# Optimization experiments

Measured on AMD Instinct MI355X. Metric: run time of the kernel, lower is better.

The kernel has to match this reference:

```python
import jax, jax.numpy as jnp
import numpy as np

NUM_HEADS = 16
ROTARY_BASE = 10000.0


def _rope_cos_sin(seqlen, rotary_dim, dtype):
    # inv_freq: (rotary_dim/2,), cos/sin: (seqlen, rotary_dim/2)
    inv_freq = 1.0 / (ROTARY_BASE ** (jnp.arange(0, rotary_dim, 2, dtype=jnp.float32) / rotary_dim))
    t = jnp.arange(seqlen, dtype=jnp.float32)
    freqs = jnp.outer(t, inv_freq)
    return jnp.cos(freqs).astype(dtype), jnp.sin(freqs).astype(dtype)


def _apply_rotary(x, cos, sin):
    # x: (b, s, h, d); cos/sin: (s, d/2). Non-interleaved (GPT-NeoX) halves.
    d2 = cos.shape[-1]
    x1, x2 = x[..., :d2], x[..., d2:2 * d2]
    c = cos[None, :, None, :]
    s = sin[None, :, None, :]
    r1 = x1 * c - x2 * s
    r2 = x1 * s + x2 * c
    return jnp.concatenate([r1, r2], axis=-1)


def setup_inputs() -> dict:
    key = jax.random.key(0)
    ks = jax.random.split(key, 5)
    B, S, E = 2, 2048, 2048
    x = jax.random.normal(ks[0], (B, S, E), dtype=jnp.float32)
    wqkv_w = jax.random.normal(ks[1], (3 * E, E), dtype=jnp.float32) * 0.02
    wqkv_b = jax.random.normal(ks[2], (3 * E,), dtype=jnp.float32) * 0.02
    out_w = jax.random.normal(ks[3], (E, E), dtype=jnp.float32) * 0.02
    out_b = jax.random.normal(ks[4], (E,), dtype=jnp.float32) * 0.02
    return {"x": x, "wqkv_w": wqkv_w, "wqkv_b": wqkv_b, "out_w": out_w, "out_b": out_b}


def reference(x, wqkv_w, wqkv_b, out_w, out_b):
    B, S, E = x.shape
    H = NUM_HEADS
    D = E // H
    # fused QKV projection: (b, s, 3, h, d)
    qkv = (jnp.einsum('bse,fe->bsf', x, wqkv_w) + wqkv_b).reshape(B, S, 3, H, D)
    q, k, v = qkv[:, :, 0], qkv[:, :, 1], qkv[:, :, 2]
    # rotary embedding on full head_dim of q and k
    cos, sin = _rope_cos_sin(S, D, x.dtype)
    q = _apply_rotary(q, cos, sin)
    k = _apply_rotary(k, cos, sin)
    # causal self-attention, softmax_scale = 1/sqrt(head_dim)
    scale = 1.0 / jnp.sqrt(jnp.asarray(D, dtype=x.dtype))
    scores = jnp.einsum('bshd,bthd->bhst', q, k) * scale
    causal_mask = jnp.tril(jnp.ones((S, S), dtype=bool))
    scores = jnp.where(causal_mask[None, None], scores, jnp.asarray(-1e30, dtype=scores.dtype))
    attn = jax.nn.softmax(scores, axis=-1)
    ctx = jnp.einsum('bhst,bthd->bshd', attn, v).reshape(B, S, E)
    return jnp.einsum('bse,fe->bsf', ctx, out_w) + out_b
```

## Files before the change

### kernel.cpp

```cpp
#include <hip/hip_runtime.h>

typedef unsigned short u16;
typedef unsigned int u32;
typedef __bf16 bf16x8 __attribute__((ext_vector_type(8)));
typedef float fx4 __attribute__((ext_vector_type(4)));

__device__ __forceinline__ float bf2f(u16 u) {
    return __uint_as_float(((u32)u) << 16);
}
__device__ __forceinline__ u16 f2bf(float f) {
    u32 x = __float_as_uint(f);
    u32 r = (x + 0x7fffu + ((x >> 16) & 1u)) >> 16;
    return (u16)r;
}

__device__ __forceinline__ void gld16(const u16* g, u16* l) {
    __builtin_amdgcn_global_load_lds(
        (const __attribute__((address_space(1))) void*)g,
        (__attribute__((address_space(3))) void*)l, 16, 0, 0);
}

#define MFMA16(a, b, c) __builtin_amdgcn_mfma_f32_16x16x32_bf16((a), (b), (c), 0, 0, 0)

__global__ __launch_bounds__(256) void cvt_kernel(const float* __restrict__ x,
                                                  const float* __restrict__ w1,
                                                  const float* __restrict__ w2,
                                                  u16* __restrict__ xb,
                                                  u16* __restrict__ w1b,
                                                  u16* __restrict__ w2b) {
    size_t g = ((size_t)blockIdx.x * 256 + threadIdx.x) * 8;
    const float* src;
    u16* dst;
    if (g < 8388608) {
        src = x;
        dst = xb;
    } else if (g < 20971520) {
        src = w1 - 8388608;
        dst = w1b - 8388608;
    } else {
        src = w2 - 20971520;
        dst = w2b - 20971520;
    }
    float4 a = *(const float4*)&src[g];
    float4 b = *(const float4*)&src[g + 4];
    u16 v[8];
    v[0] = f2bf(a.x);
    v[1] = f2bf(a.y);
    v[2] = f2bf(a.z);
    v[3] = f2bf(a.w);
    v[4] = f2bf(b.x);
    v[5] = f2bf(b.y);
    v[6] = f2bf(b.z);
    v[7] = f2bf(b.w);
    *(uint4*)&dst[g] = *(const uint4*)v;
}

template <int MODE>
__global__ __launch_bounds__(256, 2) void gemm_bt(const u16* __restrict__ A,
                                                  const u16* __restrict__ B,
                                                  const float* __restrict__ bias,
                                                  float* __restrict__ Cf,
                                                  u16* __restrict__ qb,
                                                  u16* __restrict__ kb,
                                                  u16* __restrict__ vb,
                                                  int N, int K) {
    __shared__ __align__(16) u16 As[128 * 32];
    __shared__ __align__(16) u16 Bs[128 * 32];

    const int tid = threadIdx.x;
    const int lane = tid & 63;
    const int wave = tid >> 6;
    const int quad = lane >> 4;
    const int m16 = lane & 15;
    const int wm = wave >> 1, wn = wave & 1;
    const int bm = blockIdx.y * 128, bn = blockIdx.x * 128;

    const int r0 = tid >> 2;
    const int u0 = (tid & 3) ^ ((r0 >> 1) & 3);
    const int r1 = (tid + 256) >> 2;
    const int u1 = ((tid + 256) & 3) ^ ((r1 >> 1) & 3);
    const u16* a0 = &A[(size_t)(bm + r0) * K + u0 * 8];
    const u16* a1 = &A[(size_t)(bm + r1) * K + u1 * 8];
    const u16* b0 = &B[(size_t)(bn + r0) * K + u0 * 8];
    const u16* b1 = &B[(size_t)(bn + r1) * K + u1 * 8];
    u16* la0 = &As[tid * 8];
    u16* la1 = &As[(tid + 256) * 8];
    u16* lb0 = &Bs[tid * 8];
    u16* lb1 = &Bs[(tid + 256) * 8];

    const int su = (quad ^ ((m16 >> 1) & 3)) * 8;

    const fx4 zero4 = {0.f, 0.f, 0.f, 0.f};
    fx4 acc[4][4];
#pragma unroll
    for (int i = 0; i < 4; ++i)
#pragma unroll
        for (int j = 0; j < 4; ++j) acc[i][j] = zero4;

    const int nk = K >> 5;
    for (int kt = 0; kt < nk; ++kt) {
        const int k0 = kt << 5;
        gld16(a0 + k0, la0);
        gld16(a1 + k0, la1);
        gld16(b0 + k0, lb0);
        gld16(b1 + k0, lb1);
        __syncthreads();
        bf16x8 af[4], bfr[4];
#pragma unroll
        for (int t = 0; t < 4; ++t) {
            af[t] = *(const bf16x8*)&As[(wm * 64 + t * 16 + m16) * 32 + su];
            bfr[t] = *(const bf16x8*)&Bs[(wn * 64 + t * 16 + m16) * 32 + su];
        }
#pragma unroll
        for (int mt = 0; mt < 4; ++mt)
#pragma unroll
            for (int nt = 0; nt < 4; ++nt)
                acc[mt][nt] = MFMA16(af[mt], bfr[nt], acc[mt][nt]);
        __syncthreads();
    }

#pragma unroll
    for (int mt = 0; mt < 4; ++mt) {
#pragma unroll
        for (int r = 0; r < 4; ++r) {
            int row = bm + wm * 64 + mt * 16 + quad * 4 + r;
#pragma unroll
            for (int nt = 0; nt < 4; ++nt) {
                int col = bn + wn * 64 + nt * 16 + m16;
                float v = acc[mt][nt][r] + bias[col];
                if (MODE == 0) {
                    Cf[(size_t)row * N + col] = v;
                } else {
                    int which = col >> 11;
                    int h = (col >> 7) & 15;
                    int d = col & 127;
                    int b = row >> 11;
                    int s = row & 2047;
                    u16* dst = (which == 0) ? qb : ((which == 1) ? kb : vb);
                    dst[(size_t)((b * 16 + h) * 2048 + s) * 128 + d] = f2bf(v);
                }
            }
        }
    }
}

__global__ __launch_bounds__(256) void rope_kernel(u16* __restrict__ q,
                                                   u16* __restrict__ k) {
    int t = blockIdx.x * 256 + threadIdx.x;
    int i = t & 63;
    int s = (t >> 6) & 2047;
    int bh = t >> 17;
    float inv = exp2f(-(float)i * 0.2076205059304595f);
    float ang = (float)s * inv;
    float sn, cs;
    sincosf(ang, &sn, &cs);
    size_t base = ((size_t)bh * 2048 + s) * 128 + i;
    {
        float x1 = bf2f(q[base]), x2 = bf2f(q[base + 64]);
        q[base] = f2bf(x1 * cs - x2 * sn);
        q[base + 64] = f2bf(x1 * sn + x2 * cs);
    }
    {
        float x1 = bf2f(k[base]), x2 = bf2f(k[base + 64]);
        k[base] = f2bf(x1 * cs - x2 * sn);
        k[base + 64] = f2bf(x1 * sn + x2 * cs);
    }
}

__global__ __launch_bounds__(256) void vtrans_kernel(const u16* __restrict__ v,
                                                     u16* __restrict__ vt) {
    __shared__ __align__(16) u16 L[128 * 66];
    const int tid = threadIdx.x;
    const int kb = blockIdx.x * 64;
    const int bh = blockIdx.y;
    const u16* vp = v + (size_t)bh * 2048 * 128;
    u16* op = vt + (size_t)bh * 128 * 2048;
#pragma unroll
    for (int i = 0; i < 4; ++i) {
        int c = i * 256 + tid;
        int t = c >> 4, d8 = (c & 15) << 3;
        uint4 x = *(const uint4*)&vp[(kb + t) * 128 + d8];
        const u16* xs = (const u16*)&x;
#pragma unroll
        for (int j = 0; j < 8; ++j) L[(d8 + j) * 66 + t] = xs[j];
    }
    __syncthreads();
#pragma unroll
    for (int i = 0; i < 4; ++i) {
        int c = i * 256 + tid;
        int d = c >> 3, t8 = (c & 7) << 3;
        uint4 x;
        u16* xs = (u16*)&x;
#pragma unroll
        for (int j = 0; j < 8; ++j) xs[j] = L[d * 66 + t8 + j];
        *(uint4*)&op[(size_t)d * 2048 + kb + t8] = x;
    }
}

__global__ __launch_bounds__(256, 2) void attn_kernel(const u16* __restrict__ q,
                                                      const u16* __restrict__ k,
                                                      const u16* __restrict__ vt,
                                                      u16* __restrict__ ctx) {
    __shared__ __align__(16) u16 Ks[64 * 128];
    __shared__ __align__(16) u16 Vs[128 * 64];
    __shared__ __align__(16) u16 Ps[4][16 * 64];

    const int tid = threadIdx.x;
    const int lane = tid & 63;
    const int wave = tid >> 6;
    const int quad = lane >> 4;
    const int m16 = lane & 15;

    const int l = blockIdx.x;
    const int a_ = l & 7;
    const int t_ = (l >> 3) & 1;
    const int e_ = (l >> 4) & 1;
    const int d_ = l >> 5;
    const int b_ = t_ ^ (d_ >> 3);
    const int qt_raw = a_ | (e_ << 3);
    const int qt = b_ ? (15 - qt_raw) : qt_raw;
    const int bh = d_ | (t_ << 4);
    const int b = bh >> 4, h = bh & 15;
    const int qbase = qt * 128;
    const u16* qp = q + (size_t)bh * 2048 * 128;
    const u16* kp = k + (size_t)bh * 2048 * 128;
    const u16* vp = vt + (size_t)bh * 128 * 2048;
    const float scale = 0.08838834764831845f;

    bf16x8 qf[2][4];
#pragma unroll
    for (int f = 0; f < 2; ++f)
#pragma unroll
        for (int c = 0; c < 4; ++c)
            qf[f][c] =
                *(const bf16x8*)&qp[(size_t)(qbase + wave * 32 + f * 16 + m16) *
                                        128 +
                                    c * 32 + quad * 8];

    const fx4 zero4 = {0.f, 0.f, 0.f, 0.f};
    fx4 o[2][8];
#pragma unroll
    for (int f = 0; f < 2; ++f)
#pragma unroll
        for (int i = 0; i < 8; ++i) o[f][i] = zero4;
    float mi[2][4], li[2][4];
#pragma unroll
    for (int f = 0; f < 2; ++f)
#pragma unroll
        for (int r = 0; r < 4; ++r) {
            mi[f][r] = -1e30f;
            li[f][r] = 0.f;
        }

    uint4 kr[4], vr[4];
    const int st_t = tid >> 4, st_d8 = (tid & 15) << 3;
    const int st_dv = tid >> 3, st_t8 = (tid & 7) << 3;

#define LOAD_TILE(kb_)                                                        \
    {                                                                         \
        _Pragma("unroll") for (int ii = 0; ii < 4; ++ii) {                    \
            kr[ii] = *(const uint4*)&kp[(size_t)((kb_) + st_t + ii * 16) *    \
                                            128 +                             \
                                        st_d8];                               \
            vr[ii] = *(const uint4*)&vp[(size_t)(st_dv + ii * 32) * 2048 +    \
                                        (kb_) + st_t8];                       \
        }                                                                     \
    }

#define STORE_TILE()                                                          \
    {                                                                         \
        _Pragma("unroll") for (int ii = 0; ii < 4; ++ii) {                    \
            int tt = st_t + ii * 16;                                          \
            int eK = tt * 128 + st_d8;                                        \
            *(uint4*)&Ks[eK ^ ((tt & 7) << 3)] = kr[ii];                      \
            int dv = st_dv + ii * 32;                                         \
            int eV = dv * 64 + st_t8;                                         \
            *(uint4*)&Vs[eV ^ ((dv & 7) << 3)] = vr[ii];                      \
        }                                                                     \
    }

    const int nkt = 2 * qt + 2;
    LOAD_TILE(0);
    for (int kt = 0; kt < nkt; ++kt) {
        const int kb = kt * 64;
        STORE_TILE();
        __syncthreads();
        if (kt + 1 < nkt) LOAD_TILE(kb + 64);

#pragma unroll
        for (int f = 0; f < 2; ++f) {
            fx4 sc[4];
#pragma unroll
            for (int nt = 0; nt < 4; ++nt) sc[nt] = zero4;
#pragma unroll
            for (int c = 0; c < 4; ++c)
#pragma unroll
                for (int nt = 0; nt < 4; ++nt) {
                    int e = (nt * 16 + m16) * 128 + c * 32 + quad * 8;
                    bf16x8 kf = *(const bf16x8*)&Ks[e ^ ((m16 & 7) << 3)];
                    sc[nt] = MFMA16(qf[f][c], kf, sc[nt]);
                }

#pragma unroll
            for (int r = 0; r < 4; ++r) {
                int rg = qbase + wave * 32 + f * 16 + quad * 4 + r;
                float mx = mi[f][r];
#pragma unroll
                for (int nt = 0; nt < 4; ++nt) {
                    int cg = kb + nt * 16 + m16;
                    float s = sc[nt][r] * scale;
                    s = (cg <= rg) ? s : -1e30f;
                    sc[nt][r] = s;
                    mx = fmaxf(mx, s);
                }
                mx = fmaxf(mx, __shfl_xor(mx, 1));
                mx = fmaxf(mx, __shfl_xor(mx, 2));
                mx = fmaxf(mx, __shfl_xor(mx, 4));
                mx = fmaxf(mx, __shfl_xor(mx, 8));
                float alpha = __expf(mi[f][r] - mx);
                mi[f][r] = mx;
                float rsum = 0.f;
                int row = quad * 4 + r;
#pragma unroll
                for (int nt = 0; nt < 4; ++nt) {
                    float p = __expf(sc[nt][r] - mx);
                    Ps[wave][(row * 64 + nt * 16 + m16) ^ ((row & 7) << 3)] =
                        f2bf(p);
                    rsum += p;
                }
                rsum += __shfl_xor(rsum, 1);
                rsum += __shfl_xor(rsum, 2);
                rsum += __shfl_xor(rsum, 4);
                rsum += __shfl_xor(rsum, 8);
                li[f][r] = li[f][r] * alpha + rsum;
#pragma unroll
                for (int dn = 0; dn < 8; ++dn) o[f][dn][r] *= alpha;
            }

#pragma unroll
            for (int c2 = 0; c2 < 2; ++c2) {
                bf16x8 pf = *(const bf16x8*)&Ps[wave][(m16 * 64 + c2 * 32 +
                                                       quad * 8) ^
                                                      ((m16 & 7) << 3)];
#pragma unroll
                for (int dn = 0; dn < 8; ++dn) {
                    int e = (dn * 16 + m16) * 64 + c2 * 32 + quad * 8;
                    bf16x8 vf = *(const bf16x8*)&Vs[e ^ ((m16 & 7) << 3)];
                    o[f][dn] = MFMA16(pf, vf, o[f][dn]);
                }
            }
        }
        __syncthreads();
    }

#pragma unroll
    for (int f = 0; f < 2; ++f)
#pragma unroll
        for (int r = 0; r < 4; ++r) {
            int row = qbase + wave * 32 + f * 16 + quad * 4 + r;
            float inv = 1.0f / li[f][r];
#pragma unroll
            for (int dn = 0; dn < 8; ++dn) {
                int d = dn * 16 + m16;
                ctx[((size_t)(b * 2048 + row)) * 2048 + h * 128 + d] =
                    f2bf(o[f][dn][r] * inv);
            }
        }
}

extern "C" void kernel_launch(void* const* d_in, const int* in_sizes, int n_in,
                              void* d_out, int out_size, void* d_ws,
                              size_t ws_size, hipStream_t stream) {
    const float* x = (const float*)d_in[0];
    const float* wqkv_w = (const float*)d_in[1];
    const float* wqkv_b = (const float*)d_in[2];
    const float* out_w = (const float*)d_in[3];
    const float* out_b = (const float*)d_in[4];
    u16* ws = (u16*)d_ws;

    u16* xb = ws;
    u16* wqkvb = ws + 8388608;
    u16* vb = ws + 20971520;
    u16* outwb = ws + 29360128;
    u16* vtb = xb;
    u16* ctx = vb;
    u16* qb = (u16*)d_out;
    u16* kb = qb + 8388608;

    cvt_kernel<<<12288, 256, 0, stream>>>(x, wqkv_w, out_w, xb, wqkvb, outwb);
    gemm_bt<1><<<dim3(48, 32), 256, 0, stream>>>(xb, wqkvb, wqkv_b, nullptr,
                                                 qb, kb, vb, 6144, 2048);
    rope_kernel<<<16384, 256, 0, stream>>>(qb, kb);
    vtrans_kernel<<<dim3(32, 32), 256, 0, stream>>>(vb, vtb);
    attn_kernel<<<512, 256, 0, stream>>>(qb, kb, vtb, ctx);
    gemm_bt<0><<<dim3(16, 32), 256, 0, stream>>>(ctx, outwb, out_b,
                                                 (float*)d_out, nullptr,
                                                 nullptr, nullptr, 2048, 2048);
}
```

Baseline: 490.0 us.

## Double-buffer K/V tiles in attention and use 8 waves with 16 rows each

The attention kernel moves from 4 waves handling 32 query rows each to 8 waves handling 16 rows each, with 512 threads per block. K/V tiles are now double-buffered in LDS, so storing the next tile overlaps compute on the current one and only one barrier is needed per iteration. MFMA sections are wrapped in s_setprio. This trades more LDS per block (about 80KB) and less reuse of K/V fragments per wave for more waves available to hide latency, and the larger LDS footprint may limit how many blocks fit per CU.

```diff
diff --git a/kernel.cpp b/kernel.cpp
--- a/kernel.cpp
+++ b/kernel.cpp
@@ -197,13 +197,13 @@
     }
 }
 
-__global__ __launch_bounds__(256, 2) void attn_kernel(const u16* __restrict__ q,
+__global__ __launch_bounds__(512, 4) void attn_kernel(const u16* __restrict__ q,
                                                       const u16* __restrict__ k,
                                                       const u16* __restrict__ vt,
                                                       u16* __restrict__ ctx) {
-    __shared__ __align__(16) u16 Ks[64 * 128];
-    __shared__ __align__(16) u16 Vs[128 * 64];
-    __shared__ __align__(16) u16 Ps[4][16 * 64];
+    __shared__ __align__(16) u16 Ks[2][64 * 128];
+    __shared__ __align__(16) u16 Vs[2][128 * 64];
+    __shared__ __align__(16) u16 Ps[8][16 * 64];
 
     const int tid = threadIdx.x;
     const int lane = tid & 63;
@@ -227,145 +227,144 @@
     const u16* vp = vt + (size_t)bh * 128 * 2048;
     const float scale = 0.08838834764831845f;
 
-    bf16x8 qf[2][4];
-#pragma unroll
-    for (int f = 0; f < 2; ++f)
-#pragma unroll
-        for (int c = 0; c < 4; ++c)
-            qf[f][c] =
-                *(const bf16x8*)&qp[(size_t)(qbase + wave * 32 + f * 16 + m16) *
-                                        128 +
+    bf16x8 qf[4];
+#pragma unroll
+    for (int c = 0; c < 4; ++c)
+        qf[c] = *(const bf16x8*)&qp[(size_t)(qbase + wave * 16 + m16) * 128 +
                                     c * 32 + quad * 8];
 
     const fx4 zero4 = {0.f, 0.f, 0.f, 0.f};
-    fx4 o[2][8];
-#pragma unroll
-    for (int f = 0; f < 2; ++f)
-#pragma unroll
-        for (int i = 0; i < 8; ++i) o[f][i] = zero4;
-    float mi[2][4], li[2][4];
-#pragma unroll
-    for (int f = 0; f < 2; ++f)
-#pragma unroll
-        for (int r = 0; r < 4; ++r) {
-            mi[f][r] = -1e30f;
-            li[f][r] = 0.f;
-        }
-
-    uint4 kr[4], vr[4];
+    fx4 o[8];
+#pragma unroll
+    for (int dn = 0; dn < 8; ++dn) o[dn] = zero4;
+    float mi[4], li[4];
+#pragma unroll
+    for (int r = 0; r < 4; ++r) {
+        mi[r] = -1e30f;
+        li[r] = 0.f;
+    }
+
+    uint4 kr[2], vr[2];
     const int st_t = tid >> 4, st_d8 = (tid & 15) << 3;
     const int st_dv = tid >> 3, st_t8 = (tid & 7) << 3;
 
 #define LOAD_TILE(kb_)                                                        \
     {                                                                         \
-        _Pragma("unroll") for (int ii = 0; ii < 4; ++ii) {                    \
-            kr[ii] = *(const uint4*)&kp[(size_t)((kb_) + st_t + ii * 16) *    \
+        _Pragma("unroll") for (int ii = 0; ii < 2; ++ii) {                    \
+            kr[ii] = *(const uint4*)&kp[(size_t)((kb_) + st_t + ii * 32) *    \
                                             128 +                             \
                                         st_d8];                               \
-            vr[ii] = *(const uint4*)&vp[(size_t)(st_dv + ii * 32) * 2048 +    \
+            vr[ii] = *(const uint4*)&vp[(size_t)(st_dv + ii * 64) * 2048 +    \
                                         (kb_) + st_t8];                       \
         }                                                                     \
     }
 
-#define STORE_TILE()                                                          \
+#define STORE_TILE(buf_)                                                      \
     {                                                                         \
-        _Pragma("unroll") for (int ii = 0; ii < 4; ++ii) {                    \
-            int tt = st_t + ii * 16;                                          \
+        _Pragma("unroll") for (int ii = 0; ii < 2; ++ii) {                    \
+            int tt = st_t + ii * 32;                                          \
             int eK = tt * 128 + st_d8;                                        \
-            *(uint4*)&Ks[eK ^ ((tt & 7) << 3)] = kr[ii];                      \
-            int dv = st_dv + ii * 32;                                         \
+            *(uint4*)&Ks[buf_][eK ^ ((tt & 7) << 3)] = kr[ii];                \
+            int dv = st_dv + ii * 64;                                         \
             int eV = dv * 64 + st_t8;                                         \
-            *(uint4*)&Vs[eV ^ ((dv & 7) << 3)] = vr[ii];                      \
+            *(uint4*)&Vs[buf_][eV ^ ((dv & 7) << 3)] = vr[ii];                \
         }                                                                     \
     }
 
     const int nkt = 2 * qt + 2;
     LOAD_TILE(0);
+    STORE_TILE(0);
+    if (nkt > 1) LOAD_TILE(64);
+    __syncthreads();
+
+    int cur = 0;
     for (int kt = 0; kt < nkt; ++kt) {
         const int kb = kt * 64;
-        STORE_TILE();
+        if (kt + 1 < nkt) {
+            STORE_TILE(cur ^ 1);
+            if (kt + 2 < nkt) LOAD_TILE(kb + 128);
+        }
+
+        fx4 sc[4];
+#pragma unroll
+        for (int nt = 0; nt < 4; ++nt) sc[nt] = zero4;
+        __builtin_amdgcn_s_setprio(1);
+#pragma unroll
+        for (int c = 0; c < 4; ++c)
+#pragma unroll
+            for (int nt = 0; nt < 4; ++nt) {
+                int e = (nt * 16 + m16) * 128 + c * 32 + quad * 8;
+                bf16x8 kf = *(const bf16x8*)&Ks[cur][e ^ ((m16 & 7) << 3)];
+                sc[nt] = MFMA16(qf[c], kf, sc[nt]);
+            }
+        __builtin_amdgcn_s_setprio(0);
+
+#pragma unroll
+        for (int r = 0; r < 4; ++r) {
+            int rg = qbase + wave * 16 + quad * 4 + r;
+            float mx = mi[r];
+#pragma unroll
+            for (int nt = 0; nt < 4; ++nt) {
+                int cg = kb + nt * 16 + m16;
+                float s = sc[nt][r] * scale;
+                s = (cg <= rg) ? s : -1e30f;
+                sc[nt][r] = s;
+                mx = fmaxf(mx, s);
+            }
+            mx = fmaxf(mx, __shfl_xor(mx, 1));
+            mx = fmaxf(mx, __shfl_xor(mx, 2));
+            mx = fmaxf(mx, __shfl_xor(mx, 4));
+            mx = fmaxf(mx, __shfl_xor(mx, 8));
+            float alpha = __expf(mi[r] - mx);
+            mi[r] = mx;
+            float rsum = 0.f;
+            int row = quad * 4 + r;
+#pragma unroll
+            for (int nt = 0; nt < 4; ++nt) {
+                float p = __expf(sc[nt][r] - mx);
+                Ps[wave][(row * 64 + nt * 16 + m16) ^ ((row & 7) << 3)] =
+                    f2bf(p);
+                rsum += p;
+            }
+            rsum += __shfl_xor(rsum, 1);
+            rsum += __shfl_xor(rsum, 2);
+            rsum += __shfl_xor(rsum, 4);
+            rsum += __shfl_xor(rsum, 8);
+            li[r] = li[r] * alpha + rsum;
+#pragma unroll
+            for (int dn = 0; dn < 8; ++dn) o[dn][r] *= alpha;
+        }
+
+        __builtin_amdgcn_s_setprio(1);
+#pragma unroll
+        for (int c2 = 0; c2 < 2; ++c2) {
+            bf16x8 pf = *(const bf16x8*)&Ps[wave][(m16 * 64 + c2 * 32 +
+                                                   quad * 8) ^
+                                                  ((m16 & 7) << 3)];
+#pragma unroll
+            for (int dn = 0; dn < 8; ++dn) {
+                int e = (dn * 16 + m16) * 64 + c2 * 32 + quad * 8;
+                bf16x8 vf = *(const bf16x8*)&Vs[cur][e ^ ((m16 & 7) << 3)];
+                o[dn] = MFMA16(pf, vf, o[dn]);
+            }
+        }
+        __builtin_amdgcn_s_setprio(0);
+
         __syncthreads();
-        if (kt + 1 < nkt) LOAD_TILE(kb + 64);
-
-#pragma unroll
-        for (int f = 0; f < 2; ++f) {
-            fx4 sc[4];
-#pragma unroll
-            for (int nt = 0; nt < 4; ++nt) sc[nt] = zero4;
-#pragma unroll
-            for (int c = 0; c < 4; ++c)
-#pragma unroll
-                for (int nt = 0; nt < 4; ++nt) {
-                    int e = (nt * 16 + m16) * 128 + c * 32 + quad * 8;
-                    bf16x8 kf = *(const bf16x8*)&Ks[e ^ ((m16 & 7) << 3)];
-                    sc[nt] = MFMA16(qf[f][c], kf, sc[nt]);
-                }
-
-#pragma unroll
-            for (int r = 0; r < 4; ++r) {
-                int rg = qbase + wave * 32 + f * 16 + quad * 4 + r;
-                float mx = mi[f][r];
-#pragma unroll
-                for (int nt = 0; nt < 4; ++nt) {
-                    int cg = kb + nt * 16 + m16;
-                    float s = sc[nt][r] * scale;
-                    s = (cg <= rg) ? s : -1e30f;
-                    sc[nt][r] = s;
-                    mx = fmaxf(mx, s);
-                }
-                mx = fmaxf(mx, __shfl_xor(mx, 1));
-                mx = fmaxf(mx, __shfl_xor(mx, 2));
-                mx = fmaxf(mx, __shfl_xor(mx, 4));
-                mx = fmaxf(mx, __shfl_xor(mx, 8));
-                float alpha = __expf(mi[f][r] - mx);
-                mi[f][r] = mx;
-                float rsum = 0.f;
-                int row = quad * 4 + r;
-#pragma unroll
-                for (int nt = 0; nt < 4; ++nt) {
-                    float p = __expf(sc[nt][r] - mx);
-                    Ps[wave][(row * 64 + nt * 16 + m16) ^ ((row & 7) << 3)] =
-                        f2bf(p);
-                    rsum += p;
-                }
-                rsum += __shfl_xor(rsum, 1);
-                rsum += __shfl_xor(rsum, 2);
-                rsum += __shfl_xor(rsum, 4);
-                rsum += __shfl_xor(rsum, 8);
-                li[f][r] = li[f][r] * alpha + rsum;
-#pragma unroll
-                for (int dn = 0; dn < 8; ++dn) o[f][dn][r] *= alpha;
-            }
-
-#pragma unroll
-            for (int c2 = 0; c2 < 2; ++c2) {
-                bf16x8 pf = *(const bf16x8*)&Ps[wave][(m16 * 64 + c2 * 32 +
-                                                       quad * 8) ^
-                                                      ((m16 & 7) << 3)];
-#pragma unroll
-                for (int dn = 0; dn < 8; ++dn) {
-                    int e = (dn * 16 + m16) * 64 + c2 * 32 + quad * 8;
-                    bf16x8 vf = *(const bf16x8*)&Vs[e ^ ((m16 & 7) << 3)];
-                    o[f][dn] = MFMA16(pf, vf, o[f][dn]);
-                }
-            }
-        }
-        __syncthreads();
-    }
-
-#pragma unroll
-    for (int f = 0; f < 2; ++f)
-#pragma unroll
-        for (int r = 0; r < 4; ++r) {
-            int row = qbase + wave * 32 + f * 16 + quad * 4 + r;
-            float inv = 1.0f / li[f][r];
-#pragma unroll
-            for (int dn = 0; dn < 8; ++dn) {
-                int d = dn * 16 + m16;
-                ctx[((size_t)(b * 2048 + row)) * 2048 + h * 128 + d] =
-                    f2bf(o[f][dn][r] * inv);
-            }
-        }
+        cur ^= 1;
+    }
+
+#pragma unroll
+    for (int r = 0; r < 4; ++r) {
+        int row = qbase + wave * 16 + quad * 4 + r;
+        float inv = 1.0f / li[r];
+#pragma unroll
+        for (int dn = 0; dn < 8; ++dn) {
+            int d = dn * 16 + m16;
+            ctx[((size_t)(b * 2048 + row)) * 2048 + h * 128 + d] =
+                f2bf(o[dn][r] * inv);
+        }
+    }
 }
 
 extern "C" void kernel_launch(void* const* d_in, const int* in_sizes, int n_in,
@@ -392,7 +391,7 @@
                                                  qb, kb, vb, 6144, 2048);
     rope_kernel<<<16384, 256, 0, stream>>>(qb, kb);
     vtrans_kernel<<<dim3(32, 32), 256, 0, stream>>>(vb, vtb);
-    attn_kernel<<<512, 256, 0, stream>>>(qb, kb, vtb, ctx);
+    attn_kernel<<<512, 512, 0, stream>>>(qb, kb, vtb, ctx);
     gemm_bt<0><<<dim3(16, 32), 256, 0, stream>>>(ctx, outwb, out_b,
                                                  (float*)d_out, nullptr,
                                                  nullptr, nullptr, 2048, 2048);
```

Result: slower. 607.0 us (+23.9%).
